# Kernel tuning notes

Measured on AMD Instinct MI355X. Metric: run time of the kernel, lower is better.

The kernel has to match this reference:

```python
import jax, jax.numpy as jnp
import numpy as np
import math

NH = 8   # num heads
DH = 64  # d_head = 512/8
D = 512
L = 6

def _pe(seq, d):
    pos = np.arange(seq, dtype=np.float32)[:, None]
    div = np.exp(np.arange(0, d, 2, dtype=np.float32) * (-math.log(10000.0) / d))
    pe = np.zeros((seq, d), dtype=np.float32)
    pe[:, 0::2] = np.sin(pos * div)
    pe[:, 1::2] = np.cos(pos * div)
    return jnp.asarray(pe)

def _ln(x, g, b, eps=1e-6):
    m = x.mean(-1, keepdims=True)
    v = ((x - m) ** 2).mean(-1, keepdims=True)  # unbiased=False
    return g * (x - m) / jnp.sqrt(v + eps) + b

def _mha(q_in, k_in, v_in, qkv_w, qkv_b, o_w, o_b, mask):
    b, sq, d = q_in.shape
    sk = k_in.shape[1]
    q = (q_in @ qkv_w[0] + qkv_b[0]).reshape(b, sq, NH, DH).transpose(0, 2, 1, 3)  # [b,h,sq,dh]
    k = (k_in @ qkv_w[1] + qkv_b[1]).reshape(b, sk, NH, DH).transpose(0, 2, 1, 3)
    v = (v_in @ qkv_w[2] + qkv_b[2]).reshape(b, sk, NH, DH).transpose(0, 2, 1, 3)
    scores = jnp.einsum('bhqd,bhkd->bhqk', q, k) / math.sqrt(DH)  # [b,h,sq,sk]
    if mask is not None:
        scores = jnp.where(mask, -jnp.inf, scores)  # mask True = masked, broadcast over b,h
    w = jax.nn.softmax(scores, axis=-1)
    out = jnp.einsum('bhqk,bhkd->bhqd', w, v).transpose(0, 2, 1, 3).reshape(b, sq, d)
    return out @ o_w + o_b

def _ff(x, w1, b1, w2, b2):
    return jax.nn.relu(x @ w1 + b1) @ w2 + b2

def reference(src, tgt, src_emb, tgt_emb,
              enc_qkv_w, enc_qkv_b, enc_o_w, enc_o_b,
              enc_ff_w1, enc_ff_b1, enc_ff_w2, enc_ff_b2,
              enc_ln_g, enc_ln_b, enc_fg, enc_fb,
              dec_sqkv_w, dec_sqkv_b, dec_so_w, dec_so_b,
              dec_cqkv_w, dec_cqkv_b, dec_co_w, dec_co_b,
              dec_ff_w1, dec_ff_b1, dec_ff_w2, dec_ff_b2,
              dec_ln_g, dec_ln_b, dec_fg, dec_fb):
    S, T = src.shape[1], tgt.shape[1]
    scale = math.sqrt(D)
    # ---- encoder (pre-LN) ----
    x = src_emb[src] * scale + _pe(S, D)  # [b,S,d]
    for i in range(L):
        h = _ln(x, enc_ln_g[i, 0], enc_ln_b[i, 0])
        x = x + _mha(h, h, h, enc_qkv_w[i], enc_qkv_b[i], enc_o_w[i], enc_o_b[i], None)
        h = _ln(x, enc_ln_g[i, 1], enc_ln_b[i, 1])
        x = x + _ff(h, enc_ff_w1[i], enc_ff_b1[i], enc_ff_w2[i], enc_ff_b2[i])
    memory = _ln(x, enc_fg, enc_fb)
    # ---- decoder (pre-LN) ----
    causal = jnp.triu(jnp.ones((T, T), dtype=bool), 1)  # True above diagonal = masked
    y = tgt_emb[tgt] * scale + _pe(T, D)  # [b,T,d]
    for i in range(L):
        h = _ln(y, dec_ln_g[i, 0], dec_ln_b[i, 0])
        y = y + _mha(h, h, h, dec_sqkv_w[i], dec_sqkv_b[i], dec_so_w[i], dec_so_b[i], causal)
        h = _ln(y, dec_ln_g[i, 1], dec_ln_b[i, 1])
        y = y + _mha(h, memory, memory, dec_cqkv_w[i], dec_cqkv_b[i], dec_co_w[i], dec_co_b[i], None)
        h = _ln(y, dec_ln_g[i, 2], dec_ln_b[i, 2])
        y = y + _ff(h, dec_ff_w1[i], dec_ff_b1[i], dec_ff_w2[i], dec_ff_b2[i])
    return _ln(y, dec_fg, dec_fb)

def setup_inputs():
    key = jax.random.key(0)
    ks = iter(jax.random.split(key, 40))
    B, S, T, V, DFF = 8, 128, 128, 32000, 2048
    s = 0.02
    inp = {
        'src': jax.random.randint(next(ks), (B, S), 0, V, dtype=jnp.int32),
        'tgt': jax.random.randint(next(ks), (B, T), 0, V, dtype=jnp.int32),
        'src_emb': jax.random.normal(next(ks), (V, D), jnp.float32) * s,
        'tgt_emb': jax.random.normal(next(ks), (V, D), jnp.float32) * s,
        'enc_qkv_w': jax.random.normal(next(ks), (L, 3, D, D), jnp.float32) * s,
        'enc_qkv_b': jnp.zeros((L, 3, D), jnp.float32),
        'enc_o_w': jax.random.normal(next(ks), (L, D, D), jnp.float32) * s,
        'enc_o_b': jnp.zeros((L, D), jnp.float32),
        'enc_ff_w1': jax.random.normal(next(ks), (L, D, DFF), jnp.float32) * s,
        'enc_ff_b1': jnp.zeros((L, DFF), jnp.float32),
        'enc_ff_w2': jax.random.normal(next(ks), (L, DFF, D), jnp.float32) * s,
        'enc_ff_b2': jnp.zeros((L, D), jnp.float32),
        'enc_ln_g': jnp.ones((L, 2, D), jnp.float32),
        'enc_ln_b': jnp.zeros((L, 2, D), jnp.float32),
        'enc_fg': jnp.ones((D,), jnp.float32),
        'enc_fb': jnp.zeros((D,), jnp.float32),
        'dec_sqkv_w': jax.random.normal(next(ks), (L, 3, D, D), jnp.float32) * s,
        'dec_sqkv_b': jnp.zeros((L, 3, D), jnp.float32),
        'dec_so_w': jax.random.normal(next(ks), (L, D, D), jnp.float32) * s,
        'dec_so_b': jnp.zeros((L, D), jnp.float32),
        'dec_cqkv_w': jax.random.normal(next(ks), (L, 3, D, D), jnp.float32) * s,
        'dec_cqkv_b': jnp.zeros((L, 3, D), jnp.float32),
        'dec_co_w': jax.random.normal(next(ks), (L, D, D), jnp.float32) * s,
        'dec_co_b': jnp.zeros((L, D), jnp.float32),
        'dec_ff_w1': jax.random.normal(next(ks), (L, D, DFF), jnp.float32) * s,
        'dec_ff_b1': jnp.zeros((L, DFF), jnp.float32),
        'dec_ff_w2': jax.random.normal(next(ks), (L, DFF, D), jnp.float32) * s,
        'dec_ff_b2': jnp.zeros((L, D), jnp.float32),
        'dec_ln_g': jnp.ones((L, 3, D), jnp.float32),
        'dec_ln_b': jnp.zeros((L, 3, D), jnp.float32),
        'dec_fg': jnp.ones((D,), jnp.float32),
        'dec_fb': jnp.zeros((D,), jnp.float32),
    }
    return inp
```

## Files before the change

kernel.cpp:

```cpp
#include <hip/hip_runtime.h>
#include <hip/hip_bf16.h>
#include <math.h>

#define D 512
#define NH 8
#define DHEAD 64
#define LAYERS 6
#define DFF 2048
#define BATCH 8
#define SEQ 128
#define ROWS (BATCH * SEQ)

typedef float f32x4 __attribute__((ext_vector_type(4)));
typedef short bf16x8 __attribute__((ext_vector_type(8)));

__device__ __forceinline__ unsigned short f2b(float x) {
    return __builtin_bit_cast(unsigned short, __float2bfloat16(x));
}

__global__ __launch_bounds__(256) void embed_pe_kernel(const int* __restrict__ tok,
        const float* __restrict__ emb, float* __restrict__ out)
{
    int i = blockIdx.x * 256 + threadIdx.x;
    int bs = i >> 9;
    int d  = i & 511;
    int s  = bs & (SEQ - 1);
    int tk = tok[bs];
    float dv  = expf(-(float)(d & ~1) * (9.210340371976184f / 512.0f));
    float arg = (float)s * dv;
    float pe  = (d & 1) ? cosf(arg) : sinf(arg);
    out[i] = emb[(size_t)tk * D + d] * 22.627416997969522f + pe;
}

struct TSeg { const float* src; unsigned short* dst; int cnt; };
struct TMulti { TSeg seg[6]; };

__global__ __launch_bounds__(256) void transpose_multi_kernel(TMulti m, int R, int C)
{
    __shared__ float t[32][33];
    int z = blockIdx.z, s = 0;
    while (z >= m.seg[s].cnt) { z -= m.seg[s].cnt; ++s; }
    const float* src = m.seg[s].src + (size_t)z * R * C;
    unsigned short* dst = m.seg[s].dst + (size_t)z * R * C;
    const int r0 = blockIdx.y << 5, c0 = blockIdx.x << 5;
    const int tid = threadIdx.x;
    const int rr = tid >> 3, cc = (tid & 7) << 2;
    float4 v = *(const float4*)(src + (size_t)(r0 + rr) * C + c0 + cc);
    t[rr][cc] = v.x; t[rr][cc + 1] = v.y; t[rr][cc + 2] = v.z; t[rr][cc + 3] = v.w;
    __syncthreads();
    const int oc = tid >> 3, or4 = (tid & 7) << 2;
    ushort4 o;
    o.x = f2b(t[or4 + 0][oc]);
    o.y = f2b(t[or4 + 1][oc]);
    o.z = f2b(t[or4 + 2][oc]);
    o.w = f2b(t[or4 + 3][oc]);
    *(ushort4*)(dst + (size_t)(c0 + oc) * R + r0 + or4) = o;
}

template<int OUT_BF16>
__global__ __launch_bounds__(256) void ln_kernel(const float* __restrict__ x,
        const float* __restrict__ g, const float* __restrict__ bta,
        void* __restrict__ outp)
{
    int lane = threadIdx.x & 63;
    int row  = (blockIdx.x << 2) + (threadIdx.x >> 6);
    const float* xr = x + (size_t)row * D;
    int c = lane * 8;
    float4 v0 = *(const float4*)(xr + c);
    float4 v1 = *(const float4*)(xr + c + 4);
    float s  = v0.x + v0.y + v0.z + v0.w + v1.x + v1.y + v1.z + v1.w;
    float sq = v0.x*v0.x + v0.y*v0.y + v0.z*v0.z + v0.w*v0.w
             + v1.x*v1.x + v1.y*v1.y + v1.z*v1.z + v1.w*v1.w;
    #pragma unroll
    for (int o = 32; o; o >>= 1) {
        s  += __shfl_xor(s, o);
        sq += __shfl_xor(sq, o);
    }
    float mean = s * (1.0f / D);
    float var  = sq * (1.0f / D) - mean * mean;
    float inv  = rsqrtf(var + 1e-6f);
    float4 g0 = *(const float4*)(g + c),   g1 = *(const float4*)(g + c + 4);
    float4 b0 = *(const float4*)(bta + c), b1 = *(const float4*)(bta + c + 4);
    float4 o0, o1;
    o0.x = g0.x * (v0.x - mean) * inv + b0.x;
    o0.y = g0.y * (v0.y - mean) * inv + b0.y;
    o0.z = g0.z * (v0.z - mean) * inv + b0.z;
    o0.w = g0.w * (v0.w - mean) * inv + b0.w;
    o1.x = g1.x * (v1.x - mean) * inv + b1.x;
    o1.y = g1.y * (v1.y - mean) * inv + b1.y;
    o1.z = g1.z * (v1.z - mean) * inv + b1.z;
    o1.w = g1.w * (v1.w - mean) * inv + b1.w;
    if (OUT_BF16) {
        unsigned short* orow = (unsigned short*)outp + (size_t)row * D + c;
        uint4 o;
        o.x = (unsigned int)f2b(o0.x) | ((unsigned int)f2b(o0.y) << 16);
        o.y = (unsigned int)f2b(o0.z) | ((unsigned int)f2b(o0.w) << 16);
        o.z = (unsigned int)f2b(o1.x) | ((unsigned int)f2b(o1.y) << 16);
        o.w = (unsigned int)f2b(o1.z) | ((unsigned int)f2b(o1.w) << 16);
        *(uint4*)orow = o;
    } else {
        float* orow = (float*)outp + (size_t)row * D + c;
        *(float4*)(orow)     = o0;
        *(float4*)(orow + 4) = o1;
    }
}

template<int RESID, int RELU, int OUT_BF16>
__global__ __launch_bounds__(256) void mgemm_kernel(
        const unsigned short* __restrict__ A,
        const unsigned short* __restrict__ Wt,
        const float* __restrict__ bias,
        const float* __restrict__ Rp,
        void* __restrict__ Cout,
        int N, int K,
        long aZ, long wZ, long bZ, long cZ)
{
    __shared__ unsigned short As[2][64][72];
    __shared__ unsigned short Bs[2][64][72];
    const long z = blockIdx.z;
    const unsigned short* Ab = A  + z * aZ;
    const unsigned short* Wb = Wt + z * wZ;
    const float* biasb = bias + z * bZ;
    const int tid  = threadIdx.x;
    const int lane = tid & 63, wid = tid >> 6;
    const int wm = wid >> 1, wn = wid & 1;
    const int bm = blockIdx.y << 6, bn = blockIdx.x << 6;
    const int srow = tid >> 2, sk = (tid & 3) << 4;
    const unsigned short* Ag = Ab + (size_t)(bm + srow) * K + sk;
    const unsigned short* Bg = Wb + (size_t)(bn + srow) * K + sk;
    const int fr = lane & 15;
    const int fk = (lane >> 4) << 3;
    f32x4 acc[2][2];
    #pragma unroll
    for (int i = 0; i < 2; ++i)
        #pragma unroll
        for (int j = 0; j < 2; ++j)
            acc[i][j] = (f32x4){0.f, 0.f, 0.f, 0.f};

    uint4 a0 = *(const uint4*)Ag, a1 = *(const uint4*)(Ag + 8);
    uint4 b0 = *(const uint4*)Bg, b1 = *(const uint4*)(Bg + 8);
    const int T = K >> 6;
    for (int t = 0; t < T; ++t) {
        const int p = t & 1;
        *(uint4*)&As[p][srow][sk]     = a0;
        *(uint4*)&As[p][srow][sk + 8] = a1;
        *(uint4*)&Bs[p][srow][sk]     = b0;
        *(uint4*)&Bs[p][srow][sk + 8] = b1;
        if (t + 1 < T) {
            Ag += 64; Bg += 64;
            a0 = *(const uint4*)Ag; a1 = *(const uint4*)(Ag + 8);
            b0 = *(const uint4*)Bg; b1 = *(const uint4*)(Bg + 8);
        }
        __syncthreads();
        #pragma unroll
        for (int s = 0; s < 2; ++s) {
            bf16x8 af0 = *(const bf16x8*)&As[p][wm * 32 + fr][s * 32 + fk];
            bf16x8 af1 = *(const bf16x8*)&As[p][wm * 32 + 16 + fr][s * 32 + fk];
            bf16x8 bf0 = *(const bf16x8*)&Bs[p][wn * 32 + fr][s * 32 + fk];
            bf16x8 bf1 = *(const bf16x8*)&Bs[p][wn * 32 + 16 + fr][s * 32 + fk];
            acc[0][0] = __builtin_amdgcn_mfma_f32_16x16x32_bf16(af0, bf0, acc[0][0], 0, 0, 0);
            acc[0][1] = __builtin_amdgcn_mfma_f32_16x16x32_bf16(af0, bf1, acc[0][1], 0, 0, 0);
            acc[1][0] = __builtin_amdgcn_mfma_f32_16x16x32_bf16(af1, bf0, acc[1][0], 0, 0, 0);
            acc[1][1] = __builtin_amdgcn_mfma_f32_16x16x32_bf16(af1, bf1, acc[1][1], 0, 0, 0);
        }
    }
    const int cr   = (lane >> 4) << 2;
    const int ccol = lane & 15;
    #pragma unroll
    for (int i = 0; i < 2; ++i)
        #pragma unroll
        for (int j = 0; j < 2; ++j) {
            int col = bn + wn * 32 + j * 16 + ccol;
            float bsv = biasb[col];
            #pragma unroll
            for (int r = 0; r < 4; ++r) {
                int row = bm + wm * 32 + i * 16 + cr + r;
                float v = acc[i][j][r] + bsv;
                if (RESID) v += Rp[(size_t)row * N + col];
                if (RELU)  v = fmaxf(v, 0.f);
                if (OUT_BF16) ((unsigned short*)Cout + z * cZ)[(size_t)row * N + col] = f2b(v);
                else          ((float*)Cout)[(size_t)row * N + col] = v;
            }
        }
}

template<int CAUSAL>
__device__ __forceinline__ void attn_phase(
        const unsigned short* Ks, const unsigned short* Vt,
        const unsigned short* Qs, unsigned short* Ps,
        int qbase, int brow, int hoff, unsigned short* __restrict__ Op,
        int lane, int wid)
{
    const int fr = lane & 15, fg = lane >> 4;
    f32x4 accs[8];
    #pragma unroll
    for (int kf = 0; kf < 8; ++kf) accs[kf] = (f32x4){0.f, 0.f, 0.f, 0.f};
    bf16x8 aq0 = *(const bf16x8*)&Qs[(wid * 16 + fr) * 72 + fg * 8];
    bf16x8 aq1 = *(const bf16x8*)&Qs[(wid * 16 + fr) * 72 + 32 + fg * 8];
    #pragma unroll
    for (int kf = 0; kf < 8; ++kf) {
        bf16x8 bk0 = *(const bf16x8*)&Ks[(kf * 16 + fr) * 72 + fg * 8];
        bf16x8 bk1 = *(const bf16x8*)&Ks[(kf * 16 + fr) * 72 + 32 + fg * 8];
        accs[kf] = __builtin_amdgcn_mfma_f32_16x16x32_bf16(aq0, bk0, accs[kf], 0, 0, 0);
        accs[kf] = __builtin_amdgcn_mfma_f32_16x16x32_bf16(aq1, bk1, accs[kf], 0, 0, 0);
    }
    const float SC = 0.125f * 1.44269504f;
    float linv[4];
    #pragma unroll
    for (int r = 0; r < 4; ++r) {
        int qrow = qbase + wid * 16 + fg * 4 + r;
        float sv[8];
        #pragma unroll
        for (int kf = 0; kf < 8; ++kf) {
            float s = accs[kf][r] * SC;
            if (CAUSAL) {
                int key = kf * 16 + fr;
                if (key > qrow) s = -1e30f;
            }
            sv[kf] = s;
        }
        float m = sv[0];
        #pragma unroll
        for (int kf = 1; kf < 8; ++kf) m = fmaxf(m, sv[kf]);
        #pragma unroll
        for (int o = 1; o < 16; o <<= 1) m = fmaxf(m, __shfl_xor(m, o));
        float l = 0.f;
        #pragma unroll
        for (int kf = 0; kf < 8; ++kf) {
            float p = exp2f(sv[kf] - m);
            l += p;
            Ps[(wid * 16 + fg * 4 + r) * 136 + kf * 16 + fr] = f2b(p);
        }
        #pragma unroll
        for (int o = 1; o < 16; o <<= 1) l += __shfl_xor(l, o);
        linv[r] = 1.f / l;
    }
    f32x4 acco[4];
    #pragma unroll
    for (int df = 0; df < 4; ++df) acco[df] = (f32x4){0.f, 0.f, 0.f, 0.f};
    #pragma unroll
    for (int ks = 0; ks < 4; ++ks) {
        bf16x8 pa = *(const bf16x8*)&Ps[(wid * 16 + fr) * 136 + ks * 32 + fg * 8];
        #pragma unroll
        for (int df = 0; df < 4; ++df) {
            bf16x8 vb = *(const bf16x8*)&Vt[(df * 16 + fr) * 136 + ks * 32 + fg * 8];
            acco[df] = __builtin_amdgcn_mfma_f32_16x16x32_bf16(pa, vb, acco[df], 0, 0, 0);
        }
    }
    #pragma unroll
    for (int df = 0; df < 4; ++df)
        #pragma unroll
        for (int r = 0; r < 4; ++r) {
            int qrow = qbase + wid * 16 + fg * 4 + r;
            Op[(size_t)(brow + qrow) * D + hoff + df * 16 + fr] = f2b(acco[df][r] * linv[r]);
        }
}

template<int CAUSAL>
__global__ __launch_bounds__(256) void fattn_kernel(
        const unsigned short* __restrict__ Hb,
        const unsigned short* __restrict__ W,
        const float* __restrict__ bias,
        unsigned short* __restrict__ Op)
{
    __shared__ __align__(16) char lds[63488];
    unsigned short* Ks = (unsigned short*)(lds);
    unsigned short* Vt = (unsigned short*)(lds + 18432);
    unsigned short* Qs = (unsigned short*)(lds + 35840);
    unsigned short* Ps = (unsigned short*)(lds + 46080);
    unsigned short* Hs = (unsigned short*)(lds);
    unsigned short* Ws = (unsigned short*)(lds + 18432);

    const int bh = blockIdx.x >> 1;
    const int qbase = (blockIdx.x & 1) << 6;
    const int h = bh & 7;
    const int brow = (bh >> 3) * SEQ;
    const int hoff = h * DHEAD;
    const int tid = threadIdx.x, lane = tid & 63, wid = tid >> 6;
    const int fr = lane & 15, fg = lane >> 4;

    f32x4 accK[2][4], accV[2][4], accQ[4];
    #pragma unroll
    for (int m = 0; m < 2; ++m)
        #pragma unroll
        for (int n = 0; n < 4; ++n) {
            accK[m][n] = (f32x4){0.f, 0.f, 0.f, 0.f};
            accV[m][n] = (f32x4){0.f, 0.f, 0.f, 0.f};
        }
    #pragma unroll
    for (int n = 0; n < 4; ++n) accQ[n] = (f32x4){0.f, 0.f, 0.f, 0.f};

    for (int kt = 0; kt < 8; ++kt) {
        #pragma unroll
        for (int it = 0; it < 4; ++it) {
            int idx = it * 256 + tid;
            int row = idx >> 3, c8 = (idx & 7) << 3;
            *(uint4*)&Hs[row * 72 + c8] =
                *(const uint4*)(Hb + (size_t)(brow + row) * 512 + kt * 64 + c8);
        }
        #pragma unroll
        for (int it = 0; it < 6; ++it) {
            int idx = it * 256 + tid;
            int w = idx >> 9;
            int row = (idx >> 3) & 63, c8 = (idx & 7) << 3;
            *(uint4*)&Ws[w * 4608 + row * 72 + c8] =
                *(const uint4*)(W + (size_t)(w * 512 + hoff + row) * 512 + kt * 64 + c8);
        }
        __syncthreads();
        #pragma unroll
        for (int s = 0; s < 2; ++s) {
            int fk = s * 32 + fg * 8;
            bf16x8 hm0 = *(const bf16x8*)&Hs[(wid * 32 + fr) * 72 + fk];
            bf16x8 hm1 = *(const bf16x8*)&Hs[(wid * 32 + 16 + fr) * 72 + fk];
            bf16x8 hq  = *(const bf16x8*)&Hs[(qbase + wid * 16 + fr) * 72 + fk];
            #pragma unroll
            for (int n = 0; n < 4; ++n) {
                bf16x8 wq = *(const bf16x8*)&Ws[(n * 16 + fr) * 72 + fk];
                bf16x8 wk = *(const bf16x8*)&Ws[4608 + (n * 16 + fr) * 72 + fk];
                bf16x8 wv = *(const bf16x8*)&Ws[9216 + (n * 16 + fr) * 72 + fk];
                accK[0][n] = __builtin_amdgcn_mfma_f32_16x16x32_bf16(hm0, wk, accK[0][n], 0, 0, 0);
                accK[1][n] = __builtin_amdgcn_mfma_f32_16x16x32_bf16(hm1, wk, accK[1][n], 0, 0, 0);
                accV[0][n] = __builtin_amdgcn_mfma_f32_16x16x32_bf16(hm0, wv, accV[0][n], 0, 0, 0);
                accV[1][n] = __builtin_amdgcn_mfma_f32_16x16x32_bf16(hm1, wv, accV[1][n], 0, 0, 0);
                accQ[n]    = __builtin_amdgcn_mfma_f32_16x16x32_bf16(hq,  wq, accQ[n],    0, 0, 0);
            }
        }
        __syncthreads();
    }
    #pragma unroll
    for (int m = 0; m < 2; ++m)
        #pragma unroll
        for (int n = 0; n < 4; ++n) {
            int d = n * 16 + fr;
            float bk = bias[512 + hoff + d];
            float bv = bias[1024 + hoff + d];
            #pragma unroll
            for (int r = 0; r < 4; ++r) {
                int seq = wid * 32 + m * 16 + fg * 4 + r;
                Ks[seq * 72 + d]  = f2b(accK[m][n][r] + bk);
                Vt[d * 136 + seq] = f2b(accV[m][n][r] + bv);
            }
        }
    #pragma unroll
    for (int n = 0; n < 4; ++n) {
        int d = n * 16 + fr;
        float bq = bias[hoff + d];
        #pragma unroll
        for (int r = 0; r < 4; ++r) {
            int ql = wid * 16 + fg * 4 + r;
            Qs[ql * 72 + d] = f2b(accQ[n][r] + bq);
        }
    }
    __syncthreads();
    attn_phase<CAUSAL>(Ks, Vt, Qs, Ps, qbase, brow, hoff, Op, lane, wid);
}

__global__ __launch_bounds__(256) void xattn_kernel(
        const unsigned short* __restrict__ Hb,
        const unsigned short* __restrict__ Wq,
        const float* __restrict__ bias,
        const unsigned short* __restrict__ KV,
        unsigned short* __restrict__ Op)
{
    __shared__ __align__(16) char lds[63488];
    unsigned short* Ks  = (unsigned short*)(lds);
    unsigned short* Vt  = (unsigned short*)(lds + 18432);
    unsigned short* Qs  = (unsigned short*)(lds + 35840);
    unsigned short* Ps  = (unsigned short*)(lds + 46080);
    unsigned short* Hs  = (unsigned short*)(lds + 35840);
    unsigned short* Wqs = (unsigned short*)(lds + 46080);

    const int bh = blockIdx.x >> 1;
    const int qbase = (blockIdx.x & 1) << 6;
    const int h = bh & 7;
    const int brow = (bh >> 3) * SEQ;
    const int hoff = h * DHEAD;
    const int tid = threadIdx.x, lane = tid & 63, wid = tid >> 6;
    const int fr = lane & 15, fg = lane >> 4;

    #pragma unroll
    for (int it = 0; it < 4; ++it) {
        int idx = it * 256 + tid;
        int row = idx >> 3, c8 = (idx & 7) << 3;
        const unsigned short* kvrow = KV + (size_t)(brow + row) * 1024 + hoff;
        *(uint4*)&Ks[row * 72 + c8] = *(const uint4*)(kvrow + c8);
        uint4 vu = *(const uint4*)(kvrow + 512 + c8);
        unsigned arr[4] = {vu.x, vu.y, vu.z, vu.w};
        #pragma unroll
        for (int j = 0; j < 8; ++j)
            Vt[(c8 + j) * 136 + row] = (unsigned short)(arr[j >> 1] >> ((j & 1) * 16));
    }
    f32x4 accQ[4];
    #pragma unroll
    for (int n = 0; n < 4; ++n) accQ[n] = (f32x4){0.f, 0.f, 0.f, 0.f};
    for (int kt = 0; kt < 8; ++kt) {
        #pragma unroll
        for (int it = 0; it < 2; ++it) {
            int idx = it * 256 + tid;
            int row = idx >> 3, c8 = (idx & 7) << 3;
            *(uint4*)&Hs[row * 72 + c8] =
                *(const uint4*)(Hb + (size_t)(brow + qbase + row) * 512 + kt * 64 + c8);
            *(uint4*)&Wqs[row * 72 + c8] =
                *(const uint4*)(Wq + (size_t)(hoff + row) * 512 + kt * 64 + c8);
        }
        __syncthreads();
        #pragma unroll
        for (int s = 0; s < 2; ++s) {
            int fk = s * 32 + fg * 8;
            bf16x8 hq = *(const bf16x8*)&Hs[(wid * 16 + fr) * 72 + fk];
            #pragma unroll
            for (int n = 0; n < 4; ++n) {
                bf16x8 wq = *(const bf16x8*)&Wqs[(n * 16 + fr) * 72 + fk];
                accQ[n] = __builtin_amdgcn_mfma_f32_16x16x32_bf16(hq, wq, accQ[n], 0, 0, 0);
            }
        }
        __syncthreads();
    }
    #pragma unroll
    for (int n = 0; n < 4; ++n) {
        int d = n * 16 + fr;
        float bq = bias[hoff + d];
        #pragma unroll
        for (int r = 0; r < 4; ++r) {
            int ql = wid * 16 + fg * 4 + r;
            Qs[ql * 72 + d] = f2b(accQ[n][r] + bq);
        }
    }
    __syncthreads();
    attn_phase<0>(Ks, Vt, Qs, Ps, qbase, brow, hoff, Op, lane, wid);
}

extern "C" void kernel_launch(void* const* d_in, const int* in_sizes, int n_in,
                              void* d_out, int out_size, void* d_ws, size_t ws_size,
                              hipStream_t stream)
{
    const int*   src       = (const int*)d_in[0];
    const int*   tgt       = (const int*)d_in[1];
    const float* src_emb   = (const float*)d_in[2];
    const float* tgt_emb   = (const float*)d_in[3];
    const float* enc_qkv_w = (const float*)d_in[4];
    const float* enc_qkv_b = (const float*)d_in[5];
    const float* enc_o_w   = (const float*)d_in[6];
    const float* enc_o_b   = (const float*)d_in[7];
    const float* enc_ff_w1 = (const float*)d_in[8];
    const float* enc_ff_b1 = (const float*)d_in[9];
    const float* enc_ff_w2 = (const float*)d_in[10];
    const float* enc_ff_b2 = (const float*)d_in[11];
    const float* enc_ln_g  = (const float*)d_in[12];
    const float* enc_ln_b  = (const float*)d_in[13];
    const float* enc_fg    = (const float*)d_in[14];
    const float* enc_fb    = (const float*)d_in[15];
    const float* dec_sqkv_w = (const float*)d_in[16];
    const float* dec_sqkv_b = (const float*)d_in[17];
    const float* dec_so_w   = (const float*)d_in[18];
    const float* dec_so_b   = (const float*)d_in[19];
    const float* dec_cqkv_w = (const float*)d_in[20];
    const float* dec_cqkv_b = (const float*)d_in[21];
    const float* dec_co_w   = (const float*)d_in[22];
    const float* dec_co_b   = (const float*)d_in[23];
    const float* dec_ff_w1  = (const float*)d_in[24];
    const float* dec_ff_b1  = (const float*)d_in[25];
    const float* dec_ff_w2  = (const float*)d_in[26];
    const float* dec_ff_b2  = (const float*)d_in[27];
    const float* dec_ln_g   = (const float*)d_in[28];
    const float* dec_ln_b   = (const float*)d_in[29];
    const float* dec_fg     = (const float*)d_in[30];
    const float* dec_fb     = (const float*)d_in[31];

    unsigned short* wp = (unsigned short*)d_ws;
    unsigned short* WencQKV  = wp; wp += (size_t)6 * 786432;
    unsigned short* WencO    = wp; wp += (size_t)6 * 262144;
    unsigned short* WencF1   = wp; wp += (size_t)6 * 1048576;
    unsigned short* WencF2   = wp; wp += (size_t)6 * 1048576;
    unsigned short* WdecSQKV = wp; wp += (size_t)6 * 786432;
    unsigned short* WdecSO   = wp; wp += (size_t)6 * 262144;
    unsigned short* WdecCQKV = wp; wp += (size_t)6 * 786432;
    unsigned short* WdecCO   = wp; wp += (size_t)6 * 262144;
    unsigned short* WdecF1   = wp; wp += (size_t)6 * 1048576;
    unsigned short* WdecF2   = wp; wp += (size_t)6 * 1048576;
    unsigned short* Hb   = wp; wp += ROWS * D;
    unsigned short* CKVall = wp; wp += (size_t)6 * ROWS * 1024;
    unsigned short* ATTb = wp; wp += ROWS * D;
    unsigned short* F1b  = wp; wp += ROWS * DFF;
    unsigned short* MEMb = wp; wp += ROWS * D;
    float* X = (float*)wp;

    {
        TMulti mA = {{ {enc_qkv_w,  WencQKV,  18},
                       {enc_o_w,    WencO,     6},
                       {dec_sqkv_w, WdecSQKV, 18},
                       {dec_so_w,   WdecSO,    6},
                       {dec_cqkv_w, WdecCQKV, 18},
                       {dec_co_w,   WdecCO,    6} }};
        transpose_multi_kernel<<<dim3(16, 16, 72), 256, 0, stream>>>(mA, 512, 512);
        TMulti mB = {{ {enc_ff_w1, WencF1, 6},
                       {dec_ff_w1, WdecF1, 6},
                       {nullptr, nullptr, 1 << 30}, {nullptr, nullptr, 1 << 30},
                       {nullptr, nullptr, 1 << 30}, {nullptr, nullptr, 1 << 30} }};
        transpose_multi_kernel<<<dim3(64, 16, 12), 256, 0, stream>>>(mB, 512, 2048);
        TMulti mC = {{ {enc_ff_w2, WencF2, 6},
                       {dec_ff_w2, WdecF2, 6},
                       {nullptr, nullptr, 1 << 30}, {nullptr, nullptr, 1 << 30},
                       {nullptr, nullptr, 1 << 30}, {nullptr, nullptr, 1 << 30} }};
        transpose_multi_kernel<<<dim3(16, 64, 12), 256, 0, stream>>>(mC, 2048, 512);
    }

    embed_pe_kernel<<<2048, 256, 0, stream>>>(src, src_emb, X);
    for (int i = 0; i < LAYERS; ++i) {
        ln_kernel<1><<<256, 256, 0, stream>>>(X, enc_ln_g + (size_t)(i*2+0)*D, enc_ln_b + (size_t)(i*2+0)*D, Hb);
        fattn_kernel<0><<<128, 256, 0, stream>>>(Hb, WencQKV + (size_t)i*786432,
                enc_qkv_b + (size_t)i*1536, ATTb);
        mgemm_kernel<1,0,0><<<dim3(8,16,1), 256, 0, stream>>>(ATTb, WencO + (size_t)i*262144,
                enc_o_b + (size_t)i*512, X, X, 512, 512, 0, 0, 0, 0);
        ln_kernel<1><<<256, 256, 0, stream>>>(X, enc_ln_g + (size_t)(i*2+1)*D, enc_ln_b + (size_t)(i*2+1)*D, Hb);
        mgemm_kernel<0,1,1><<<dim3(32,16,1), 256, 0, stream>>>(Hb, WencF1 + (size_t)i*1048576,
                enc_ff_b1 + (size_t)i*DFF, nullptr, F1b, DFF, 512, 0, 0, 0, 0);
        mgemm_kernel<1,0,0><<<dim3(8,16,1), 256, 0, stream>>>(F1b, WencF2 + (size_t)i*1048576,
                enc_ff_b2 + (size_t)i*512, X, X, 512, DFF, 0, 0, 0, 0);
    }
    ln_kernel<1><<<256, 256, 0, stream>>>(X, enc_fg, enc_fb, MEMb);

    mgemm_kernel<0,0,1><<<dim3(16,16,6), 256, 0, stream>>>(MEMb, WdecCQKV + 262144,
            dec_cqkv_b + 512, nullptr, CKVall, 1024, 512,
            0, 786432, 1536, (long)ROWS * 1024);

    embed_pe_kernel<<<2048, 256, 0, stream>>>(tgt, tgt_emb, X);
    for (int i = 0; i < LAYERS; ++i) {
        ln_kernel<1><<<256, 256, 0, stream>>>(X, dec_ln_g + (size_t)(i*3+0)*D, dec_ln_b + (size_t)(i*3+0)*D, Hb);
        fattn_kernel<1><<<128, 256, 0, stream>>>(Hb, WdecSQKV + (size_t)i*786432,
                dec_sqkv_b + (size_t)i*1536, ATTb);
        mgemm_kernel<1,0,0><<<dim3(8,16,1), 256, 0, stream>>>(ATTb, WdecSO + (size_t)i*262144,
                dec_so_b + (size_t)i*512, X, X, 512, 512, 0, 0, 0, 0);
        ln_kernel<1><<<256, 256, 0, stream>>>(X, dec_ln_g + (size_t)(i*3+1)*D, dec_ln_b + (size_t)(i*3+1)*D, Hb);
        xattn_kernel<<<128, 256, 0, stream>>>(Hb, WdecCQKV + (size_t)i*786432,
                dec_cqkv_b + (size_t)i*1536, CKVall + (size_t)i*ROWS*1024, ATTb);
        mgemm_kernel<1,0,0><<<dim3(8,16,1), 256, 0, stream>>>(ATTb, WdecCO + (size_t)i*262144,
                dec_co_b + (size_t)i*512, X, X, 512, 512, 0, 0, 0, 0);
        ln_kernel<1><<<256, 256, 0, stream>>>(X, dec_ln_g + (size_t)(i*3+2)*D, dec_ln_b + (size_t)(i*3+2)*D, Hb);
        mgemm_kernel<0,1,1><<<dim3(32,16,1), 256, 0, stream>>>(Hb, WdecF1 + (size_t)i*1048576,
                dec_ff_b1 + (size_t)i*DFF, nullptr, F1b, DFF, 512, 0, 0, 0, 0);
        mgemm_kernel<1,0,0><<<dim3(8,16,1), 256, 0, stream>>>(F1b, WdecF2 + (size_t)i*1048576,
                dec_ff_b2 + (size_t)i*512, X, X, 512, DFF, 0, 0, 0, 0);
    }
    ln_kernel<0><<<256, 256, 0, stream>>>(X, dec_fg, dec_fb, d_out);
}
```

Baseline: 804.8 us.

## Unfuse self-attention QKV projection into a separate GEMM plus attention kernel

```diff
diff --git a/kernel.cpp b/kernel.cpp
--- a/kernel.cpp
+++ b/kernel.cpp
@@ -18,9 +18,15 @@
     return __builtin_bit_cast(unsigned short, __float2bfloat16(x));
 }
 
-__global__ __launch_bounds__(256) void embed_pe_kernel(const int* __restrict__ tok,
-        const float* __restrict__ emb, float* __restrict__ out)
-{
+__global__ __launch_bounds__(256) void embed_pe_kernel(
+        const int* __restrict__ tok0, const int* __restrict__ tok1,
+        const float* __restrict__ emb0, const float* __restrict__ emb1,
+        float* __restrict__ out0, float* __restrict__ out1)
+{
+    const int z = blockIdx.z;
+    const int* tok = z ? tok1 : tok0;
+    const float* emb = z ? emb1 : emb0;
+    float* out = z ? out1 : out0;
     int i = blockIdx.x * 256 + threadIdx.x;
     int bs = i >> 9;
     int d  = i & 511;
@@ -257,99 +263,42 @@
 }
 
 template<int CAUSAL>
-__global__ __launch_bounds__(256) void fattn_kernel(
-        const unsigned short* __restrict__ Hb,
-        const unsigned short* __restrict__ W,
-        const float* __restrict__ bias,
+__global__ __launch_bounds__(256) void attn_kernel(
+        const unsigned short* __restrict__ Qp, int qs,
+        const unsigned short* __restrict__ Kp,
+        const unsigned short* __restrict__ Vp, int kvs,
         unsigned short* __restrict__ Op)
 {
-    __shared__ __align__(16) char lds[63488];
-    unsigned short* Ks = (unsigned short*)(lds);
-    unsigned short* Vt = (unsigned short*)(lds + 18432);
-    unsigned short* Qs = (unsigned short*)(lds + 35840);
-    unsigned short* Ps = (unsigned short*)(lds + 46080);
-    unsigned short* Hs = (unsigned short*)(lds);
-    unsigned short* Ws = (unsigned short*)(lds + 18432);
-
-    const int bh = blockIdx.x >> 1;
+    __shared__ unsigned short Ks[128 * 72];
+    __shared__ unsigned short Qs[64 * 72];
+    __shared__ unsigned short Vt[64 * 136];
+    __shared__ unsigned short Ps[64 * 136];
+    const int bh    = blockIdx.x >> 1;
     const int qbase = (blockIdx.x & 1) << 6;
-    const int h = bh & 7;
-    const int brow = (bh >> 3) * SEQ;
-    const int hoff = h * DHEAD;
+    const int brow  = (bh >> 3) * SEQ;
+    const int hoff  = (bh & 7) * DHEAD;
     const int tid = threadIdx.x, lane = tid & 63, wid = tid >> 6;
-    const int fr = lane & 15, fg = lane >> 4;
-
-    f32x4 accK[2][4], accV[2][4], accQ[4];
-    #pragma unroll
-    for (int m = 0; m < 2; ++m)
-        #pragma unroll
-        for (int n = 0; n < 4; ++n) {
-            accK[m][n] = (f32x4){0.f, 0.f, 0.f, 0.f};
-            accV[m][n] = (f32x4){0.f, 0.f, 0.f, 0.f};
-        }
-    #pragma unroll
-    for (int n = 0; n < 4; ++n) accQ[n] = (f32x4){0.f, 0.f, 0.f, 0.f};
-
-    for (int kt = 0; kt < 8; ++kt) {
-        #pragma unroll
-        for (int it = 0; it < 4; ++it) {
-            int idx = it * 256 + tid;
-            int row = idx >> 3, c8 = (idx & 7) << 3;
-            *(uint4*)&Hs[row * 72 + c8] =
-                *(const uint4*)(Hb + (size_t)(brow + row) * 512 + kt * 64 + c8);
-        }
-        #pragma unroll
-        for (int it = 0; it < 6; ++it) {
-            int idx = it * 256 + tid;
-            int w = idx >> 9;
-            int row = (idx >> 3) & 63, c8 = (idx & 7) << 3;
-            *(uint4*)&Ws[w * 4608 + row * 72 + c8] =
-                *(const uint4*)(W + (size_t)(w * 512 + hoff + row) * 512 + kt * 64 + c8);
-        }
-        __syncthreads();
-        #pragma unroll
-        for (int s = 0; s < 2; ++s) {
-            int fk = s * 32 + fg * 8;
-            bf16x8 hm0 = *(const bf16x8*)&Hs[(wid * 32 + fr) * 72 + fk];
-            bf16x8 hm1 = *(const bf16x8*)&Hs[(wid * 32 + 16 + fr) * 72 + fk];
-            bf16x8 hq  = *(const bf16x8*)&Hs[(qbase + wid * 16 + fr) * 72 + fk];
-            #pragma unroll
-            for (int n = 0; n < 4; ++n) {
-                bf16x8 wq = *(const bf16x8*)&Ws[(n * 16 + fr) * 72 + fk];
-                bf16x8 wk = *(const bf16x8*)&Ws[4608 + (n * 16 + fr) * 72 + fk];
-                bf16x8 wv = *(const bf16x8*)&Ws[9216 + (n * 16 + fr) * 72 + fk];
-                accK[0][n] = __builtin_amdgcn_mfma_f32_16x16x32_bf16(hm0, wk, accK[0][n], 0, 0, 0);
-                accK[1][n] = __builtin_amdgcn_mfma_f32_16x16x32_bf16(hm1, wk, accK[1][n], 0, 0, 0);
-                accV[0][n] = __builtin_amdgcn_mfma_f32_16x16x32_bf16(hm0, wv, accV[0][n], 0, 0, 0);
-                accV[1][n] = __builtin_amdgcn_mfma_f32_16x16x32_bf16(hm1, wv, accV[1][n], 0, 0, 0);
-                accQ[n]    = __builtin_amdgcn_mfma_f32_16x16x32_bf16(hq,  wq, accQ[n],    0, 0, 0);
-            }
-        }
-        __syncthreads();
-    }
-    #pragma unroll
-    for (int m = 0; m < 2; ++m)
-        #pragma unroll
-        for (int n = 0; n < 4; ++n) {
-            int d = n * 16 + fr;
-            float bk = bias[512 + hoff + d];
-            float bv = bias[1024 + hoff + d];
-            #pragma unroll
-            for (int r = 0; r < 4; ++r) {
-                int seq = wid * 32 + m * 16 + fg * 4 + r;
-                Ks[seq * 72 + d]  = f2b(accK[m][n][r] + bk);
-                Vt[d * 136 + seq] = f2b(accV[m][n][r] + bv);
-            }
-        }
-    #pragma unroll
-    for (int n = 0; n < 4; ++n) {
-        int d = n * 16 + fr;
-        float bq = bias[hoff + d];
-        #pragma unroll
-        for (int r = 0; r < 4; ++r) {
-            int ql = wid * 16 + fg * 4 + r;
-            Qs[ql * 72 + d] = f2b(accQ[n][r] + bq);
-        }
+
+    #pragma unroll
+    for (int it = 0; it < 4; ++it) {
+        int idx = it * 256 + tid;
+        int row = idx >> 3;
+        int c8  = (idx & 7) << 3;
+        *(uint4*)&Ks[row * 72 + c8] =
+            *(const uint4*)(Kp + (size_t)(brow + row) * kvs + hoff + c8);
+        uint4 vu = *(const uint4*)(Vp + (size_t)(brow + row) * kvs + hoff + c8);
+        unsigned arr[4] = {vu.x, vu.y, vu.z, vu.w};
+        #pragma unroll
+        for (int j = 0; j < 8; ++j)
+            Vt[(c8 + j) * 136 + row] = (unsigned short)(arr[j >> 1] >> ((j & 1) * 16));
+    }
+    #pragma unroll
+    for (int it = 0; it < 2; ++it) {
+        int idx = it * 256 + tid;
+        int row = idx >> 3;
+        int c8  = (idx & 7) << 3;
+        *(uint4*)&Qs[row * 72 + c8] =
+            *(const uint4*)(Qp + (size_t)(brow + qbase + row) * qs + hoff + c8);
     }
     __syncthreads();
     attn_phase<CAUSAL>(Ks, Vt, Qs, Ps, qbase, brow, hoff, Op, lane, wid);
@@ -479,11 +428,13 @@
     unsigned short* WdecF1   = wp; wp += (size_t)6 * 1048576;
     unsigned short* WdecF2   = wp; wp += (size_t)6 * 1048576;
     unsigned short* Hb   = wp; wp += ROWS * D;
+    unsigned short* QKVb = wp; wp += ROWS * 3 * D;
     unsigned short* CKVall = wp; wp += (size_t)6 * ROWS * 1024;
     unsigned short* ATTb = wp; wp += ROWS * D;
     unsigned short* F1b  = wp; wp += ROWS * DFF;
     unsigned short* MEMb = wp; wp += ROWS * D;
-    float* X = (float*)wp;
+    float* X  = (float*)wp;  wp += ROWS * D * 2;
+    float* X2 = (float*)wp;  wp += ROWS * D * 2;
 
     {
         TMulti mA = {{ {enc_qkv_w,  WencQKV,  18},
@@ -505,11 +456,13 @@
         transpose_multi_kernel<<<dim3(16, 64, 12), 256, 0, stream>>>(mC, 2048, 512);
     }
 
-    embed_pe_kernel<<<2048, 256, 0, stream>>>(src, src_emb, X);
+    embed_pe_kernel<<<dim3(2048, 1, 2), 256, 0, stream>>>(src, tgt, src_emb, tgt_emb, X, X2);
+
     for (int i = 0; i < LAYERS; ++i) {
         ln_kernel<1><<<256, 256, 0, stream>>>(X, enc_ln_g + (size_t)(i*2+0)*D, enc_ln_b + (size_t)(i*2+0)*D, Hb);
-        fattn_kernel<0><<<128, 256, 0, stream>>>(Hb, WencQKV + (size_t)i*786432,
-                enc_qkv_b + (size_t)i*1536, ATTb);
+        mgemm_kernel<0,0,1><<<dim3(24,16,1), 256, 0, stream>>>(Hb, WencQKV + (size_t)i*786432,
+                enc_qkv_b + (size_t)i*1536, nullptr, QKVb, 1536, 512, 0, 0, 0, 0);
+        attn_kernel<0><<<128, 256, 0, stream>>>(QKVb, 1536, QKVb + 512, QKVb + 1024, 1536, ATTb);
         mgemm_kernel<1,0,0><<<dim3(8,16,1), 256, 0, stream>>>(ATTb, WencO + (size_t)i*262144,
                 enc_o_b + (size_t)i*512, X, X, 512, 512, 0, 0, 0, 0);
         ln_kernel<1><<<256, 256, 0, stream>>>(X, enc_ln_g + (size_t)(i*2+1)*D, enc_ln_b + (size_t)(i*2+1)*D, Hb);
@@ -524,23 +477,23 @@
             dec_cqkv_b + 512, nullptr, CKVall, 1024, 512,
             0, 786432, 1536, (long)ROWS * 1024);
 
-    embed_pe_kernel<<<2048, 256, 0, stream>>>(tgt, tgt_emb, X);
     for (int i = 0; i < LAYERS; ++i) {
-        ln_kernel<1><<<256, 256, 0, stream>>>(X, dec_ln_g + (size_t)(i*3+0)*D, dec_ln_b + (size_t)(i*3+0)*D, Hb);
-        fattn_kernel<1><<<128, 256, 0, stream>>>(Hb, WdecSQKV + (size_t)i*786432,
-                dec_sqkv_b + (size_t)i*1536, ATTb);
+        ln_kernel<1><<<256, 256, 0, stream>>>(X2, dec_ln_g + (size_t)(i*3+0)*D, dec_ln_b + (size_t)(i*3+0)*D, Hb);
+        mgemm_kernel<0,0,1><<<dim3(24,16,1), 256, 0, stream>>>(Hb, WdecSQKV + (size_t)i*786432,
+                dec_sqkv_b + (size_t)i*1536, nullptr, QKVb, 1536, 512, 0, 0, 0, 0);
+        attn_kernel<1><<<128, 256, 0, stream>>>(QKVb, 1536, QKVb + 512, QKVb + 1024, 1536, ATTb);
         mgemm_kernel<1,0,0><<<dim3(8,16,1), 256, 0, stream>>>(ATTb, WdecSO + (size_t)i*262144,
-                dec_so_b + (size_t)i*512, X, X, 512, 512, 0, 0, 0, 0);
-        ln_kernel<1><<<256, 256, 0, stream>>>(X, dec_ln_g + (size_t)(i*3+1)*D, dec_ln_b + (size_t)(i*3+1)*D, Hb);
+                dec_so_b + (size_t)i*512, X2, X2, 512, 512, 0, 0, 0, 0);
+        ln_kernel<1><<<256, 256, 0, stream>>>(X2, dec_ln_g + (size_t)(i*3+1)*D, dec_ln_b + (size_t)(i*3+1)*D, Hb);
         xattn_kernel<<<128, 256, 0, stream>>>(Hb, WdecCQKV + (size_t)i*786432,
                 dec_cqkv_b + (size_t)i*1536, CKVall + (size_t)i*ROWS*1024, ATTb);
         mgemm_kernel<1,0,0><<<dim3(8,16,1), 256, 0, stream>>>(ATTb, WdecCO + (size_t)i*262144,
-                dec_co_b + (size_t)i*512, X, X, 512, 512, 0, 0, 0, 0);
-        ln_kernel<1><<<256, 256, 0, stream>>>(X, dec_ln_g + (size_t)(i*3+2)*D, dec_ln_b + (size_t)(i*3+2)*D, Hb);
+                dec_co_b + (size_t)i*512, X2, X2, 512, 512, 0, 0, 0, 0);
+        ln_kernel<1><<<256, 256, 0, stream>>>(X2, dec_ln_g + (size_t)(i*3+2)*D, dec_ln_b + (size_t)(i*3+2)*D, Hb);
         mgemm_kernel<0,1,1><<<dim3(32,16,1), 256, 0, stream>>>(Hb, WdecF1 + (size_t)i*1048576,
                 dec_ff_b1 + (size_t)i*DFF, nullptr, F1b, DFF, 512, 0, 0, 0, 0);
         mgemm_kernel<1,0,0><<<dim3(8,16,1), 256, 0, stream>>>(F1b, WdecF2 + (size_t)i*1048576,
-                dec_ff_b2 + (size_t)i*512, X, X, 512, DFF, 0, 0, 0, 0);
-    }
-    ln_kernel<0><<<256, 256, 0, stream>>>(X, dec_fg, dec_fb, d_out);
-}
+                dec_ff_b2 + (size_t)i*512, X2, X2, 512, DFF, 0, 0, 0, 0);
+    }
+    ln_kernel<0><<<256, 256, 0, stream>>>(X2, dec_fg, dec_fb, d_out);
+}
```

New measurement: 750.4 us, median of 3. -6.8%, faster.
